# Kernel optimization log

Hardware: AMD Instinct MI355X
Metric: run time of the kernel (lower is better)

## Reference

```python
import jax, jax.numpy as jnp
import numpy as np

B, D, E, H, C, TOPK = 4096, 768, 16, 768, 1000, 4

def setup_inputs() -> dict:
    key = jax.random.key(0)
    ks = jax.random.split(key, 4)
    s_in = 1.0 / np.sqrt(D)
    return {
        'features': jax.random.normal(ks[0], (B, D), dtype=jnp.float32),
        'router_w': jax.random.normal(ks[1], (D, E), dtype=jnp.float32) * s_in,
        'router_b': jnp.zeros((E,), jnp.float32),
        'ln_g': jnp.ones((E, D), jnp.float32),
        'ln_b': jnp.zeros((E, D), jnp.float32),
        'w1': jax.random.normal(ks[2], (E, D, H), dtype=jnp.float32) * s_in,
        'b1': jnp.zeros((E, H), jnp.float32),
        'w2': jax.random.normal(ks[3], (E, H, C), dtype=jnp.float32) * (1.0 / np.sqrt(H)),
        'b2': jnp.zeros((E, C), jnp.float32),
    }

def reference(features, router_w, router_b, ln_g, ln_b, w1, b1, w2, b2):
    # router
    gate_logits = features @ router_w + router_b          # [B,E]
    gate_probs = jax.nn.softmax(gate_logits, axis=-1)
    topk_vals, topk_idx = jax.lax.top_k(gate_probs, TOPK)  # [B,K]
    topk_vals = topk_vals / jnp.sum(topk_vals, axis=-1, keepdims=True)

    # all experts computed densely: LayerNorm (per-expert affine) -> Linear -> GELU -> Linear
    mu = jnp.mean(features, axis=-1, keepdims=True)
    var = jnp.mean((features - mu) ** 2, axis=-1, keepdims=True)
    xn = (features - mu) / jnp.sqrt(var + 1e-5)            # [B,D]
    y = xn[:, None, :] * ln_g[None, :, :] + ln_b[None, :, :]  # [B,E,D]
    h = jax.nn.gelu(jnp.einsum('bed,edh->beh', y, w1) + b1[None], approximate=False)  # [B,E,H]
    all_logits = jnp.einsum('beh,ehc->bec', h, w2) + b2[None]  # [B,E,C]

    # top-k gather + weighted softmax mixture
    selected = jnp.take_along_axis(all_logits, topk_idx[:, :, None], axis=1)  # [B,K,C]
    market_probs = jnp.sum(topk_vals[:, :, None] * jax.nn.softmax(selected, axis=-1), axis=1)  # [B,C]
    all_probs = jax.nn.softmax(jnp.transpose(all_logits, (1, 0, 2)), axis=-1)  # [E,B,C]
    return market_probs, all_probs, gate_probs
```

## Files before the change

### kernel.cpp

```cpp
#include <hip/hip_runtime.h>
#include <hip/hip_bf16.h>
#include <cmath>

#define B_ 4096
#define D_ 768
#define E_ 16
#define H_ 768
#define C_ 1000
#define CP_ 1024
#define K_ 768

typedef __bf16 bf16_t;
typedef __bf16 bf16x8 __attribute__((ext_vector_type(8)));
typedef float f32x4 __attribute__((ext_vector_type(4)));

__device__ __forceinline__ void async_lds16(const void* g, void* l) {
  __builtin_amdgcn_global_load_lds(
      (const __attribute__((address_space(1))) void*)g,
      (__attribute__((address_space(3))) void*)l, 16, 0, 0);
}

__global__ __launch_bounds__(256) void k_router_ln(
    const float* __restrict__ feat, const float* __restrict__ rw,
    const float* __restrict__ rb, float* __restrict__ gate_out,
    int* __restrict__ tk_idx, float* __restrict__ tk_val,
    bf16_t* __restrict__ xn) {
  int w = threadIdx.x >> 6, lane = threadIdx.x & 63;
  int b = blockIdx.x * 4 + w;
  float acc[E_];
#pragma unroll
  for (int e = 0; e < E_; ++e) acc[e] = 0.f;
  const float* frow = feat + (size_t)b * D_;
  float v[D_ / 64];
  float s = 0.f, sq = 0.f;
#pragma unroll
  for (int it = 0; it < D_ / 64; ++it) {
    int d = it * 64 + lane;
    float f = frow[d];
    v[it] = f; s += f; sq += f * f;
    const float4* r4 = reinterpret_cast<const float4*>(rw + (size_t)d * E_);
    float4 q0 = r4[0], q1 = r4[1], q2 = r4[2], q3 = r4[3];
    acc[0]  += f * q0.x; acc[1]  += f * q0.y; acc[2]  += f * q0.z; acc[3]  += f * q0.w;
    acc[4]  += f * q1.x; acc[5]  += f * q1.y; acc[6]  += f * q1.z; acc[7]  += f * q1.w;
    acc[8]  += f * q2.x; acc[9]  += f * q2.y; acc[10] += f * q2.z; acc[11] += f * q2.w;
    acc[12] += f * q3.x; acc[13] += f * q3.y; acc[14] += f * q3.z; acc[15] += f * q3.w;
  }
#pragma unroll
  for (int off = 32; off; off >>= 1) { s += __shfl_xor(s, off); sq += __shfl_xor(sq, off); }
  float mu = s * (1.f / D_);
  float var = sq * (1.f / D_) - mu * mu;
  float rs = rsqrtf(var + 1e-5f);
  bf16_t* o = xn + (size_t)b * D_;
#pragma unroll
  for (int it = 0; it < D_ / 64; ++it)
    o[it * 64 + lane] = (bf16_t)((v[it] - mu) * rs);
#pragma unroll
  for (int e = 0; e < E_; ++e) {
#pragma unroll
    for (int off = 32; off; off >>= 1) acc[e] += __shfl_xor(acc[e], off);
    acc[e] += rb[e];
  }
  if (lane == 0) {
    float mx = acc[0];
#pragma unroll
    for (int e = 1; e < E_; ++e) mx = fmaxf(mx, acc[e]);
    float p[E_]; float ps = 0.f;
#pragma unroll
    for (int e = 0; e < E_; ++e) { p[e] = expf(acc[e] - mx); ps += p[e]; }
    float inv = 1.f / ps;
    float* go = gate_out + (size_t)b * E_;
#pragma unroll
    for (int e = 0; e < E_; ++e) { p[e] *= inv; go[e] = p[e]; }
    float lg[E_];
#pragma unroll
    for (int e = 0; e < E_; ++e) lg[e] = acc[e];
    int idx4[4]; float v4[4]; float vs = 0.f;
#pragma unroll
    for (int k = 0; k < 4; ++k) {
      int bi = 0; float bv = -1e30f;
#pragma unroll
      for (int e = 0; e < E_; ++e) { if (lg[e] > bv) { bv = lg[e]; bi = e; } }
      idx4[k] = bi; v4[k] = p[bi]; vs += p[bi]; lg[bi] = -1e30f;
    }
    float nv = 1.f / vs;
#pragma unroll
    for (int k = 0; k < 4; ++k) { tk_idx[b * 4 + k] = idx4[k]; tk_val[b * 4 + k] = v4[k] * nv; }
  }
}

__global__ __launch_bounds__(256) void k_bias_init(const float* __restrict__ b1,
                                                   float* __restrict__ bias1) {
  int i = blockIdx.x * 256 + threadIdx.x;
  bias1[i] = b1[i];
}

__global__ void k_tw1(const float* __restrict__ w1, const float* __restrict__ lng,
                      const float* __restrict__ lnb, bf16_t* __restrict__ w1T,
                      float* __restrict__ bias1) {
  __shared__ float t[32][33];
  __shared__ float br[8][33];
  int e = blockIdx.z, dT = blockIdx.y * 32, hT = blockIdx.x * 32;
  int tx = threadIdx.x, ty = threadIdx.y;
  const float* w1e = w1 + (size_t)e * D_ * H_;
  const float* ge = lng + (size_t)e * D_;
  const float* lb = lnb + (size_t)e * D_;
  float bsum = 0.f;
#pragma unroll
  for (int r = 0; r < 4; ++r) {
    int d = dT + ty + r * 8;
    float val = w1e[(size_t)d * H_ + hT + tx];
    t[ty + r * 8][tx] = val * ge[d];
    bsum += lb[d] * val;
  }
  br[ty][tx] = bsum;
  __syncthreads();
  bf16_t* o = w1T + (size_t)e * H_ * D_;
#pragma unroll
  for (int r = 0; r < 4; ++r) {
    int h = hT + ty + r * 8;
    o[(size_t)h * D_ + dT + tx] = (bf16_t)t[tx][ty + r * 8];
  }
  if (ty == 0) {
    float a = 0.f;
#pragma unroll
    for (int z = 0; z < 8; ++z) a += br[z][tx];
    atomicAdd(&bias1[(size_t)e * H_ + hT + tx], a);
  }
}

__global__ void k_tw2(const float* __restrict__ w2, bf16_t* __restrict__ w2T) {
  __shared__ float t[32][33];
  int e = blockIdx.z, hT = blockIdx.y * 32, cT = blockIdx.x * 32;
  int tx = threadIdx.x, ty = threadIdx.y;
  const float* w2e = w2 + (size_t)e * H_ * C_;
#pragma unroll
  for (int r = 0; r < 4; ++r) {
    int h = hT + ty + r * 8, c = cT + tx;
    t[ty + r * 8][tx] = (c < C_) ? w2e[(size_t)h * C_ + c] : 0.f;
  }
  __syncthreads();
  bf16_t* o = w2T + (size_t)e * CP_ * H_;
#pragma unroll
  for (int r = 0; r < 4; ++r) {
    int c = cT + ty + r * 8;
    o[(size_t)c * H_ + hT + tx] = (bf16_t)t[tx][ty + r * 8];
  }
}

template <int MODE, int NT>
__global__ __launch_bounds__(256) void k_gemm(
    const bf16_t* __restrict__ Abase, size_t aStride,
    const bf16_t* __restrict__ Bt, int Np,
    const float* __restrict__ bias,
    bf16_t* __restrict__ outb, float* __restrict__ outf) {
  __shared__ __attribute__((aligned(16))) bf16_t As[128 * 32];
  __shared__ __attribute__((aligned(16))) bf16_t Bs[128 * 32];
  int id = blockIdx.x;
  int xcd = id & 7, seq = id >> 3;
  const int PER_E = 32 * NT;
  int e = xcd * (E_ / 8) + seq / PER_E;
  int rem = seq % PER_E;
  int m0 = (rem / NT) * 128, n0 = (rem % NT) * 128;

  const bf16_t* A = Abase + (size_t)e * aStride;
  const bf16_t* Be = Bt + ((size_t)e * Np + n0) * K_;
  int tid = threadIdx.x;
  int lane = tid & 63, w = tid >> 6;
  int wm = (w & 1) * 64, wn = (w >> 1) * 64;
  int fr = lane & 15, fk = (lane >> 4) * 8;

  f32x4 acc[4][4];
#pragma unroll
  for (int i = 0; i < 4; ++i)
#pragma unroll
    for (int j = 0; j < 4; ++j) acc[i][j] = f32x4{0.f, 0.f, 0.f, 0.f};

  int r0 = tid >> 2;
  int c0 = (tid & 3) * 8;
  const bf16_t* a_src0 = A + (size_t)(m0 + r0) * K_ + c0;
  const bf16_t* a_src1 = A + (size_t)(m0 + r0 + 64) * K_ + c0;
  const bf16_t* b_src0 = Be + (size_t)r0 * K_ + c0;
  const bf16_t* b_src1 = Be + (size_t)(r0 + 64) * K_ + c0;
  bf16_t* a_dst0 = As + tid * 8;
  bf16_t* a_dst1 = As + 2048 + tid * 8;
  bf16_t* b_dst0 = Bs + tid * 8;
  bf16_t* b_dst1 = Bs + 2048 + tid * 8;

  for (int kk = 0; kk < K_; kk += 32) {
    async_lds16(a_src0 + kk, a_dst0);
    async_lds16(a_src1 + kk, a_dst1);
    async_lds16(b_src0 + kk, b_dst0);
    async_lds16(b_src1 + kk, b_dst1);
    __syncthreads();
    bf16x8 afr[4], bfr[4];
#pragma unroll
    for (int i = 0; i < 4; ++i)
      afr[i] = *(const bf16x8*)&As[(wm + i * 16 + fr) * 32 + fk];
#pragma unroll
    for (int i = 0; i < 4; ++i)
      bfr[i] = *(const bf16x8*)&Bs[(wn + i * 16 + fr) * 32 + fk];
#pragma unroll
    for (int i = 0; i < 4; ++i)
#pragma unroll
      for (int j = 0; j < 4; ++j)
        acc[i][j] = __builtin_amdgcn_mfma_f32_16x16x32_bf16(afr[i], bfr[j], acc[i][j], 0, 0, 0);
    __syncthreads();
  }

  int rbse = (lane >> 4) * 4;
  int cl = lane & 15;
#pragma unroll
  for (int i = 0; i < 4; ++i) {
#pragma unroll
    for (int j = 0; j < 4; ++j) {
      int n = n0 + wn + j * 16 + cl;
      if (MODE == 0) {
        float bs = bias[(size_t)e * H_ + n];
#pragma unroll
        for (int r = 0; r < 4; ++r) {
          int m = m0 + wm + i * 16 + rbse + r;
          float vv = acc[i][j][r] + bs;
          vv = 0.5f * vv * (1.f + erff(vv * 0.70710678118654752f));
          outb[((size_t)e * B_ + m) * H_ + n] = (bf16_t)vv;
        }
      } else if (MODE == 1) {
        float bs = (n < C_) ? bias[(size_t)e * C_ + n] : 0.f;
#pragma unroll
        for (int r = 0; r < 4; ++r) {
          int m = m0 + wm + i * 16 + rbse + r;
          outb[((size_t)e * B_ + m) * CP_ + n] = (bf16_t)(acc[i][j][r] + bs);
        }
      } else {
        if (n < C_) {
          float bs = bias[(size_t)e * C_ + n];
#pragma unroll
          for (int r = 0; r < 4; ++r) {
            int m = m0 + wm + i * 16 + rbse + r;
            outf[((size_t)e * B_ + m) * C_ + n] = acc[i][j][r] + bs;
          }
        }
      }
    }
  }
}

__global__ __launch_bounds__(256) void k_softmax_b(const bf16_t* __restrict__ lg,
                                                   float* __restrict__ out1) {
  int w = threadIdx.x >> 6, lane = threadIdx.x & 63;
  size_t r = (size_t)blockIdx.x * 4 + w;
  const bf16_t* row = lg + r * CP_;
  float f[2][8];
  float mx = -1e30f;
#pragma unroll
  for (int it = 0; it < 2; ++it) {
    int ch = it * 64 + lane;
    bf16x8 x = *(const bf16x8*)(row + ch * 8);
    if (ch < 125) {
#pragma unroll
      for (int q = 0; q < 8; ++q) { f[it][q] = (float)x[q]; mx = fmaxf(mx, f[it][q]); }
    }
  }
#pragma unroll
  for (int off = 32; off; off >>= 1) mx = fmaxf(mx, __shfl_xor(mx, off));
  float s = 0.f;
#pragma unroll
  for (int it = 0; it < 2; ++it) {
    int ch = it * 64 + lane;
    if (ch < 125) {
#pragma unroll
      for (int q = 0; q < 8; ++q) { f[it][q] = __expf(f[it][q] - mx); s += f[it][q]; }
    }
  }
#pragma unroll
  for (int off = 32; off; off >>= 1) s += __shfl_xor(s, off);
  float inv = 1.f / s;
  float* orow = out1 + r * C_;
#pragma unroll
  for (int it = 0; it < 2; ++it) {
    int ch = it * 64 + lane;
    if (ch < 125) {
      float4 a = make_float4(f[it][0] * inv, f[it][1] * inv, f[it][2] * inv, f[it][3] * inv);
      float4 b = make_float4(f[it][4] * inv, f[it][5] * inv, f[it][6] * inv, f[it][7] * inv);
      *(float4*)(orow + ch * 8) = a;
      *(float4*)(orow + ch * 8 + 4) = b;
    }
  }
}

__global__ __launch_bounds__(256) void k_softmax(float* __restrict__ p) {
  int w = threadIdx.x >> 6, lane = threadIdx.x & 63;
  size_t r = (size_t)blockIdx.x * 4 + w;
  float* row = p + r * C_;
  float4* row4 = reinterpret_cast<float4*>(row);
  const int n4 = C_ / 4;
  float4 v[4];
  float mx = -1e30f;
#pragma unroll
  for (int i = 0; i < 4; ++i) {
    int idx = i * 64 + lane;
    if (idx < n4) {
      v[i] = row4[idx];
      mx = fmaxf(mx, fmaxf(fmaxf(v[i].x, v[i].y), fmaxf(v[i].z, v[i].w)));
    }
  }
#pragma unroll
  for (int off = 32; off; off >>= 1) mx = fmaxf(mx, __shfl_xor(mx, off));
  float s = 0.f;
#pragma unroll
  for (int i = 0; i < 4; ++i) {
    int idx = i * 64 + lane;
    if (idx < n4) {
      v[i].x = __expf(v[i].x - mx); v[i].y = __expf(v[i].y - mx);
      v[i].z = __expf(v[i].z - mx); v[i].w = __expf(v[i].w - mx);
      s += v[i].x + v[i].y + v[i].z + v[i].w;
    }
  }
#pragma unroll
  for (int off = 32; off; off >>= 1) s += __shfl_xor(s, off);
  float inv = 1.f / s;
#pragma unroll
  for (int i = 0; i < 4; ++i) {
    int idx = i * 64 + lane;
    if (idx < n4) {
      v[i].x *= inv; v[i].y *= inv; v[i].z *= inv; v[i].w *= inv;
      row4[idx] = v[i];
    }
  }
}

__global__ __launch_bounds__(256) void k_market(const float* __restrict__ allp,
                                                const int* __restrict__ tki,
                                                const float* __restrict__ tkv,
                                                float* __restrict__ out0) {
  int b = blockIdx.y;
  int c = blockIdx.x * 256 + threadIdx.x;
  if (c >= C_) return;
  const int* ix = tki + (size_t)b * 4;
  const float* vv = tkv + (size_t)b * 4;
  float s = 0.f;
#pragma unroll
  for (int k = 0; k < 4; ++k)
    s += vv[k] * allp[((size_t)ix[k] * B_ + b) * C_ + c];
  out0[(size_t)b * C_ + c] = s;
}

extern "C" void kernel_launch(void* const* d_in, const int* in_sizes, int n_in,
                              void* d_out, int out_size, void* d_ws, size_t ws_size,
                              hipStream_t stream) {
  const float* feat = (const float*)d_in[0];
  const float* rw   = (const float*)d_in[1];
  const float* rb   = (const float*)d_in[2];
  const float* lng  = (const float*)d_in[3];
  const float* lnb  = (const float*)d_in[4];
  const float* w1   = (const float*)d_in[5];
  const float* b1   = (const float*)d_in[6];
  const float* w2   = (const float*)d_in[7];
  const float* b2   = (const float*)d_in[8];

  float* out0 = (float*)d_out;
  float* out1 = out0 + (size_t)B_ * C_;
  float* out2 = out1 + (size_t)E_ * B_ * C_;

  char* ws = (char*)d_ws;
  size_t off = 0;
  auto take = [&](size_t bytes) -> void* {
    void* p = ws + off;
    off += (bytes + 255) & ~(size_t)255;
    return p;
  };
  bf16_t* xn   = (bf16_t*)take((size_t)B_ * D_ * 2);
  bf16_t* w1T  = (bf16_t*)take((size_t)E_ * H_ * D_ * 2);
  bf16_t* w2T  = (bf16_t*)take((size_t)E_ * CP_ * H_ * 2);
  float* bias1 = (float*)take((size_t)E_ * H_ * 4);
  int* tki     = (int*)take((size_t)B_ * 4 * 4);
  float* tkv   = (float*)take((size_t)B_ * 4 * 4);
  bf16_t* Hact = (bf16_t*)take((size_t)E_ * B_ * H_ * 2);
  size_t logit_bytes = (size_t)E_ * B_ * CP_ * 2;
  bool use_b16_logits = (off + logit_bytes) <= ws_size;
  bf16_t* logitsB = use_b16_logits ? (bf16_t*)take(logit_bytes) : nullptr;

  k_router_ln<<<B_ / 4, 256, 0, stream>>>(feat, rw, rb, out2, tki, tkv, xn);
  k_bias_init<<<E_ * H_ / 256, 256, 0, stream>>>(b1, bias1);
  k_tw1<<<dim3(24, 24, E_), dim3(32, 8), 0, stream>>>(w1, lng, lnb, w1T, bias1);
  k_tw2<<<dim3(32, 24, E_), dim3(32, 8), 0, stream>>>(w2, w2T);
  k_gemm<0, 6><<<E_ * 32 * 6, 256, 0, stream>>>(xn, 0, w1T, H_, bias1, Hact, nullptr);
  if (use_b16_logits) {
    k_gemm<1, 8><<<E_ * 32 * 8, 256, 0, stream>>>(Hact, (size_t)B_ * H_, w2T, CP_, b2, logitsB, nullptr);
    k_softmax_b<<<(E_ * B_) / 4, 256, 0, stream>>>(logitsB, out1);
  } else {
    k_gemm<2, 8><<<E_ * 32 * 8, 256, 0, stream>>>(Hact, (size_t)B_ * H_, w2T, CP_, b2, nullptr, out1);
    k_softmax<<<(E_ * B_) / 4, 256, 0, stream>>>(out1);
  }
  k_market<<<dim3(4, B_), 256, 0, stream>>>(out1, tki, tkv, out0);
}
```

Baseline: 708.7 us.

## Replace 128x128 GEMM with 256x256 double-buffered swizzled-LDS GEMM kernel

Replaces the per-expert bf16 MFMA GEMM with a 512-thread kernel that computes 256x256 output tiles over a K-step of 64. LDS is double-buffered with async global-to-LDS loads and a partial vmcnt wait, so the next tile's loads overlap the current MFMAs. LDS columns are XOR-swizzled to avoid bank conflicts, and s_setprio is raised around the MFMA bursts. The intent is more operand reuse per byte loaded and less load latency exposed per iteration. The cost is 128 KB of LDS per block and more accumulator registers, which limits occupancy.

```diff
diff --git a/kernel.cpp b/kernel.cpp
--- a/kernel.cpp
+++ b/kernel.cpp
@@ -147,78 +147,121 @@
   }
 }
 
-template <int MODE, int NT>
-__global__ __launch_bounds__(256) void k_gemm(
+template <int MODE>
+__global__ __launch_bounds__(512, 2) void k_gemm256(
     const bf16_t* __restrict__ Abase, size_t aStride,
     const bf16_t* __restrict__ Bt, int Np,
     const float* __restrict__ bias,
     bf16_t* __restrict__ outb, float* __restrict__ outf) {
-  __shared__ __attribute__((aligned(16))) bf16_t As[128 * 32];
-  __shared__ __attribute__((aligned(16))) bf16_t Bs[128 * 32];
+  __shared__ __attribute__((aligned(16))) bf16_t smbuf[2][2][256 * 64];
   int id = blockIdx.x;
   int xcd = id & 7, seq = id >> 3;
-  const int PER_E = 32 * NT;
-  int e = xcd * (E_ / 8) + seq / PER_E;
-  int rem = seq % PER_E;
-  int m0 = (rem / NT) * 128, n0 = (rem % NT) * 128;
-
-  const bf16_t* A = Abase + (size_t)e * aStride;
-  const bf16_t* Be = Bt + ((size_t)e * Np + n0) * K_;
+  int e, m0, n0;
+  if (MODE == 0) {
+    int m = seq / 6, rr = seq % 6;
+    e = xcd * 2 + rr / 3;
+    m0 = m * 256;
+    n0 = (rr % 3) * 256;
+  } else {
+    e = xcd * 2 + (seq >> 6);
+    int rr = seq & 63;
+    m0 = (rr >> 2) * 256;
+    n0 = (rr & 3) * 256;
+  }
+  const bf16_t* A = Abase + (size_t)e * aStride + (size_t)m0 * K_;
+  const bf16_t* Bp = Bt + ((size_t)e * Np + n0) * K_;
+
   int tid = threadIdx.x;
-  int lane = tid & 63, w = tid >> 6;
-  int wm = (w & 1) * 64, wn = (w >> 1) * 64;
-  int fr = lane & 15, fk = (lane >> 4) * 8;
-
-  f32x4 acc[4][4];
-#pragma unroll
-  for (int i = 0; i < 4; ++i)
+  int lane = tid & 63;
+  int wid = tid >> 6;
+  int wm = wid >> 2, wn = wid & 3;
+  int fr = lane & 15, hi = lane >> 4;
+  int sw0 = (hi ^ (fr & 7)) * 8;
+
+  int srow = tid >> 3;
+  int scg = (tid & 7) ^ (srow & 7);
+  const bf16_t* asrc = A + (size_t)srow * K_ + scg * 8;
+  const bf16_t* bsrc = Bp + (size_t)srow * K_ + scg * 8;
+
+  f32x4 acc[8][4];
+#pragma unroll
+  for (int i = 0; i < 8; ++i)
 #pragma unroll
     for (int j = 0; j < 4; ++j) acc[i][j] = f32x4{0.f, 0.f, 0.f, 0.f};
 
-  int r0 = tid >> 2;
-  int c0 = (tid & 3) * 8;
-  const bf16_t* a_src0 = A + (size_t)(m0 + r0) * K_ + c0;
-  const bf16_t* a_src1 = A + (size_t)(m0 + r0 + 64) * K_ + c0;
-  const bf16_t* b_src0 = Be + (size_t)r0 * K_ + c0;
-  const bf16_t* b_src1 = Be + (size_t)(r0 + 64) * K_ + c0;
-  bf16_t* a_dst0 = As + tid * 8;
-  bf16_t* a_dst1 = As + 2048 + tid * 8;
-  bf16_t* b_dst0 = Bs + tid * 8;
-  bf16_t* b_dst1 = Bs + 2048 + tid * 8;
-
-  for (int kk = 0; kk < K_; kk += 32) {
-    async_lds16(a_src0 + kk, a_dst0);
-    async_lds16(a_src1 + kk, a_dst1);
-    async_lds16(b_src0 + kk, b_dst0);
-    async_lds16(b_src1 + kk, b_dst1);
-    __syncthreads();
-    bf16x8 afr[4], bfr[4];
-#pragma unroll
-    for (int i = 0; i < 4; ++i)
-      afr[i] = *(const bf16x8*)&As[(wm + i * 16 + fr) * 32 + fk];
-#pragma unroll
-    for (int i = 0; i < 4; ++i)
-      bfr[i] = *(const bf16x8*)&Bs[(wn + i * 16 + fr) * 32 + fk];
-#pragma unroll
-    for (int i = 0; i < 4; ++i)
-#pragma unroll
-      for (int j = 0; j < 4; ++j)
-        acc[i][j] = __builtin_amdgcn_mfma_f32_16x16x32_bf16(afr[i], bfr[j], acc[i][j], 0, 0, 0);
-    __syncthreads();
-  }
-
-  int rbse = (lane >> 4) * 4;
-  int cl = lane & 15;
-#pragma unroll
-  for (int i = 0; i < 4; ++i) {
+  auto STAGE = [&](int kt, int nb) {
+    bf16_t* ad = &smbuf[nb][0][tid * 8];
+    bf16_t* bd = &smbuf[nb][1][tid * 8];
+    const bf16_t* as = asrc + kt * 64;
+    const bf16_t* bs = bsrc + kt * 64;
+#pragma unroll
+    for (int s = 0; s < 4; ++s) {
+      async_lds16(as + (size_t)s * 64 * K_, ad + s * 4096);
+      async_lds16(bs + (size_t)s * 64 * K_, bd + s * 4096);
+    }
+  };
+
+  bf16x8 af[4][2], bfr[2][2];
+  auto COMPUTE = [&](int cur) {
+    const bf16_t* Ala = &smbuf[cur][0][(wm * 128 + fr) * 64];
+    const bf16_t* Bla = &smbuf[cur][1][(wn * 64 + fr) * 64];
+#pragma unroll
+    for (int q = 0; q < 4; ++q) {
+      const int mq = q >> 1;
+      const int nq = (q == 1 || q == 2);
+      if (q == 0 || q == 2) {
+#pragma unroll
+        for (int i = 0; i < 4; ++i)
+#pragma unroll
+          for (int ks = 0; ks < 2; ++ks)
+            af[i][ks] = *(const bf16x8*)&Ala[(mq * 64 + i * 16) * 64 + (sw0 ^ (ks * 32))];
+      }
+      if (q != 2) {
+#pragma unroll
+        for (int j = 0; j < 2; ++j)
+#pragma unroll
+          for (int ks = 0; ks < 2; ++ks)
+            bfr[j][ks] = *(const bf16x8*)&Bla[(nq * 32 + j * 16) * 64 + (sw0 ^ (ks * 32))];
+      }
+      __builtin_amdgcn_s_barrier();
+      __builtin_amdgcn_s_setprio(1);
+#pragma unroll
+      for (int i = 0; i < 4; ++i)
+#pragma unroll
+        for (int j = 0; j < 2; ++j)
+#pragma unroll
+          for (int ks = 0; ks < 2; ++ks)
+            acc[mq * 4 + i][nq * 2 + j] = __builtin_amdgcn_mfma_f32_16x16x32_bf16(
+                af[i][ks], bfr[j][ks], acc[mq * 4 + i][nq * 2 + j], 0, 0, 0);
+      __builtin_amdgcn_s_setprio(0);
+      __builtin_amdgcn_s_barrier();
+    }
+  };
+
+  constexpr int NKT = K_ / 64;
+  STAGE(0, 0);
+  for (int t = 0; t < NKT - 1; ++t) {
+    STAGE(t + 1, (t + 1) & 1);
+    asm volatile("s_waitcnt vmcnt(8)" ::: "memory");
+    __builtin_amdgcn_s_barrier();
+    COMPUTE(t & 1);
+  }
+  asm volatile("s_waitcnt vmcnt(0)" ::: "memory");
+  __builtin_amdgcn_s_barrier();
+  COMPUTE((NKT - 1) & 1);
+
+  int rb = hi * 4;
+  int cl = fr;
+#pragma unroll
+  for (int i = 0; i < 8; ++i) {
 #pragma unroll
     for (int j = 0; j < 4; ++j) {
-      int n = n0 + wn + j * 16 + cl;
+      int n = n0 + wn * 64 + j * 16 + cl;
       if (MODE == 0) {
         float bs = bias[(size_t)e * H_ + n];
 #pragma unroll
         for (int r = 0; r < 4; ++r) {
-          int m = m0 + wm + i * 16 + rbse + r;
+          int m = m0 + wm * 128 + i * 16 + rb + r;
           float vv = acc[i][j][r] + bs;
           vv = 0.5f * vv * (1.f + erff(vv * 0.70710678118654752f));
           outb[((size_t)e * B_ + m) * H_ + n] = (bf16_t)vv;
@@ -227,7 +270,7 @@
         float bs = (n < C_) ? bias[(size_t)e * C_ + n] : 0.f;
 #pragma unroll
         for (int r = 0; r < 4; ++r) {
-          int m = m0 + wm + i * 16 + rbse + r;
+          int m = m0 + wm * 128 + i * 16 + rb + r;
           outb[((size_t)e * B_ + m) * CP_ + n] = (bf16_t)(acc[i][j][r] + bs);
         }
       } else {
@@ -235,7 +278,7 @@
           float bs = bias[(size_t)e * C_ + n];
 #pragma unroll
           for (int r = 0; r < 4; ++r) {
-            int m = m0 + wm + i * 16 + rbse + r;
+            int m = m0 + wm * 128 + i * 16 + rb + r;
             outf[((size_t)e * B_ + m) * C_ + n] = acc[i][j][r] + bs;
           }
         }
@@ -383,12 +426,12 @@
   k_bias_init<<<E_ * H_ / 256, 256, 0, stream>>>(b1, bias1);
   k_tw1<<<dim3(24, 24, E_), dim3(32, 8), 0, stream>>>(w1, lng, lnb, w1T, bias1);
   k_tw2<<<dim3(32, 24, E_), dim3(32, 8), 0, stream>>>(w2, w2T);
-  k_gemm<0, 6><<<E_ * 32 * 6, 256, 0, stream>>>(xn, 0, w1T, H_, bias1, Hact, nullptr);
+  k_gemm256<0><<<E_ * 16 * 3, 512, 0, stream>>>(xn, 0, w1T, H_, bias1, Hact, nullptr);
   if (use_b16_logits) {
-    k_gemm<1, 8><<<E_ * 32 * 8, 256, 0, stream>>>(Hact, (size_t)B_ * H_, w2T, CP_, b2, logitsB, nullptr);
+    k_gemm256<1><<<E_ * 16 * 4, 512, 0, stream>>>(Hact, (size_t)B_ * H_, w2T, CP_, b2, logitsB, nullptr);
     k_softmax_b<<<(E_ * B_) / 4, 256, 0, stream>>>(logitsB, out1);
   } else {
-    k_gemm<2, 8><<<E_ * 32 * 8, 256, 0, stream>>>(Hact, (size_t)B_ * H_, w2T, CP_, b2, nullptr, out1);
+    k_gemm256<2><<<E_ * 16 * 4, 512, 0, stream>>>(Hact, (size_t)B_ * H_, w2T, CP_, b2, nullptr, out1);
     k_softmax<<<(E_ * B_) / 4, 256, 0, stream>>>(out1);
   }
   k_market<<<dim3(4, B_), 256, 0, stream>>>(out1, tki, tkv, out0);
```

Result: no change. 703.4 us (-0.7%).
